# Optimization experiments

Hardware: AMD Instinct MI355X
Metric: run time of the kernel (lower is better)

## Reference

```python
import jax, jax.numpy as jnp
import numpy as np

R, DIL = 3, 2  # radius, dilation for neighbor correlation


def conv2d(x, w, b):
    # standard 3x3 stride-1 SAME conv, NCHW / OIHW
    y = jax.lax.conv_general_dilated(x, w, (1, 1), 'SAME',
                                     dimension_numbers=('NCHW', 'OIHW', 'NCHW'))
    return y + b[None, :, None, None]


def bilinear_gather(x, py, px):
    # x: (n,c,h,w); py/px: (n,K,h,w) float sampling coords; zero outside bounds
    n, c, h, w = x.shape
    y0 = jnp.floor(py); x0 = jnp.floor(px)
    wy = py - y0; wx = px - x0
    xf = x.reshape(n, c, h * w)

    def gather(yi, xi):
        valid = ((yi >= 0) & (yi < h) & (xi >= 0) & (xi < w)).astype(x.dtype)
        yc = jnp.clip(yi, 0, h - 1).astype(jnp.int32)
        xc = jnp.clip(xi, 0, w - 1).astype(jnp.int32)
        idx = (yc * w + xc).reshape(n, -1)  # (n, K*h*w)
        v = jax.vmap(lambda f, i: f[:, i])(xf, idx)  # (n, c, K*h*w)
        return v.reshape(n, c, *yi.shape[1:]) * valid[:, None]

    v00 = gather(y0, x0); v01 = gather(y0, x0 + 1)
    v10 = gather(y0 + 1, x0); v11 = gather(y0 + 1, x0 + 1)
    wy_ = wy[:, None]; wx_ = wx[:, None]
    return (v00 * (1 - wy_) * (1 - wx_) + v01 * (1 - wy_) * wx_
            + v10 * wy_ * (1 - wx_) + v11 * wy_ * wx_)


def dcn(x, w, b, ow, ob):
    # DCNv2-style modulated deformable 3x3 conv, stride 1, pad 1, 1 deformable group.
    # Offset/mask predicted by an internal conv: channels = [dy(9), dx(9), mask(9)].
    n, c, h, w_ = x.shape
    K = 9
    om = conv2d(x, ow, ob)  # (n, 27, h, w)
    dy, dx = om[:, :K], om[:, K:2 * K]
    mask = jax.nn.sigmoid(om[:, 2 * K:])
    ky, kx = jnp.meshgrid(jnp.arange(-1, 2), jnp.arange(-1, 2), indexing='ij')
    ky = ky.reshape(K).astype(x.dtype); kx = kx.reshape(K).astype(x.dtype)
    yy = jnp.arange(h, dtype=x.dtype)[None, None, :, None]
    xx = jnp.arange(w_, dtype=x.dtype)[None, None, None, :]
    py = yy + ky[None, :, None, None] + dy  # (n,K,h,w)
    px = xx + kx[None, :, None, None] + dx
    samp = bilinear_gather(x, py, px) * mask[:, None]  # (n,c,K,h,w)
    return jnp.einsum('nckhw,ock->nohw', samp, w.reshape(w.shape[0], c, K)) + b[None, :, None, None]


def ncf(f1, f2, radius, dilation):
    # neighbor_correlation_filter: unfold-based sliding-window dot-product attention
    n, c, h, w = f2.shape
    k = 2 * radius + 1
    pad = (k - 1) * dilation // 2
    f2p = jnp.pad(f2, ((0, 0), (0, 0), (pad, pad), (pad, pad)))
    # (n,c,K,h,w), tap order (ky outer, kx inner) matching F.unfold row-major layout
    patches = jnp.stack([f2p[:, :, i * dilation:i * dilation + h, j * dilation:j * dilation + w]
                         for i in range(k) for j in range(k)], axis=2)
    corr = jnp.einsum('nchw,nckhw->nkhw', f1, patches) / jnp.sqrt(jnp.asarray(c, f1.dtype))
    attn = jax.nn.softmax(corr, axis=1)
    sample = jnp.einsum('nkhw,nckhw->nchw', attn, patches)
    return sample, corr


def stargru(x, t, zw, zb, zow, zob, hw, hb, how, hob):
    tx = jnp.concatenate([x, t], axis=1)
    z = jax.nn.sigmoid(dcn(tx, zw, zb, zow, zob))
    r, _ = ncf(t, x, R, DIL)
    xt = jnp.tanh(dcn(jnp.concatenate([r, t], axis=1), hw, hb, how, hob))
    return (1.0 - z) * t + z * xt


def setup_inputs():
    key = jax.random.key(0)
    N, CIN, CH, H, W = 2, 256, 64, 96, 96
    ks = iter(jax.random.split(key, 32))

    def rn(shape, s=0.05):
        return jax.random.normal(next(ks), shape, jnp.float32) * s

    inp = {
        'x': jax.random.normal(next(ks), (N, CIN, H, W), jnp.float32),
        'template': jax.random.normal(next(ks), (N, CH, H, W), jnp.float32),
        'w_in': rn((CH, CIN, 3, 3)), 'b_in': jnp.zeros((CH,), jnp.float32),
        'w_out': rn((CIN, CH, 3, 3)), 'b_out': jnp.zeros((CIN,), jnp.float32),
    }
    for pre in ('enh_z', 'enh_h', 'upd_z', 'upd_h'):
        inp[pre + '_w'] = rn((CH, 2 * CH, 3, 3))
        inp[pre + '_b'] = jnp.zeros((CH,), jnp.float32)
        inp[pre + '_ow'] = rn((27, 2 * CH, 3, 3), 0.01)  # offset/mask conv (small init)
        inp[pre + '_ob'] = jnp.zeros((27,), jnp.float32)
    return inp


def reference(x, template, w_in, b_in, w_out, b_out,
              enh_z_w, enh_z_b, enh_z_ow, enh_z_ob,
              enh_h_w, enh_h_b, enh_h_ow, enh_h_ob,
              upd_z_w, upd_z_b, upd_z_ow, upd_z_ob,
              upd_h_w, upd_h_b, upd_h_ow, upd_h_ob):
    # CrossUpdate forward, post-first-frame branch (self.template is not None)
    xh = conv2d(x, w_in, b_in)
    x_enh = stargru(template, xh,
                    enh_z_w, enh_z_b, enh_z_ow, enh_z_ob,
                    enh_h_w, enh_h_b, enh_h_ow, enh_h_ob)
    new_template = stargru(xh, template,
                           upd_z_w, upd_z_b, upd_z_ow, upd_z_ob,
                           upd_h_w, upd_h_b, upd_h_ow, upd_h_ob)
    out = conv2d(x_enh, w_out, b_out)
    return (out, new_template)
```

## Files before the change

### kernel.cpp

```cpp
#include <hip/hip_runtime.h>
#include <hip/hip_bf16.h>

typedef __hip_bfloat16 bf16;
typedef unsigned short u16;
typedef unsigned int u32;
typedef __attribute__((ext_vector_type(8))) short short8;
typedef __attribute__((ext_vector_type(4))) short bh4;
typedef __attribute__((ext_vector_type(4))) float floatx4;

constexpr int N_ = 2, H_ = 96, W_ = 96, HW_ = H_ * W_;
constexpr int CIN_ = 256, CH_ = 64, C2_ = 128;

__device__ __forceinline__ float sigm(float v) { return 1.0f / (1.0f + __expf(-v)); }
__device__ __forceinline__ short f2b(float v) { bf16 h = __float2bfloat16(v); return *reinterpret_cast<short*>(&h); }
__device__ __forceinline__ float b2f(short s) {
    union { u32 i; float f; } v; v.i = ((u32)(u16)s) << 16; return v.f;
}

constexpr int A_IN_OFF = 0,                         A_IN_SZ  = 64 * 2304;
constexpr int A_OUT_OFF = A_IN_OFF + A_IN_SZ,       A_OUT_SZ = 256 * 576;
constexpr int A_OFF_OFF = A_OUT_OFF + A_OUT_SZ,     A_OFF_SZ = 64 * 1152;
constexpr int A_DCN_OFF = A_OFF_OFF + 4 * A_OFF_SZ, A_DCN_SZ = 64 * 1152;
constexpr int A_TOT = A_DCN_OFF + 4 * A_DCN_SZ;

__global__ __launch_bounds__(256) void cvt_weights(
        const float* __restrict__ w_in, const float* __restrict__ w_out,
        const float* __restrict__ ow0, const float* __restrict__ ow1,
        const float* __restrict__ ow2, const float* __restrict__ ow3,
        const float* __restrict__ w0, const float* __restrict__ w1,
        const float* __restrict__ w2, const float* __restrict__ w3,
        u16* __restrict__ dst) {
    int id = blockIdx.x * 256 + threadIdx.x;
    if (id >= A_TOT) return;
    float v;
    if (id < A_OUT_OFF) {
        int l = id; int m = l / 2304, k = l % 2304; int tap = k >> 8, ic = k & 255;
        v = w_in[m * 2304 + ic * 9 + tap];
    } else if (id < A_OFF_OFF) {
        int l = id - A_OUT_OFF; int m = l / 576, k = l % 576; int tap = k / 64, ic = k & 63;
        v = w_out[m * 576 + ic * 9 + tap];
    } else if (id < A_DCN_OFF) {
        int l = id - A_OFF_OFF; int i = l / A_OFF_SZ, l2 = l % A_OFF_SZ;
        int m = l2 / 1152, k = l2 % 1152; int tap = k >> 7, ic = k & 127;
        const float* s = (i == 0) ? ow0 : (i == 1) ? ow1 : (i == 2) ? ow2 : ow3;
        v = (m < 27) ? s[m * 1152 + ic * 9 + tap] : 0.f;
    } else {
        int l = id - A_DCN_OFF; int i = l / A_DCN_SZ, l2 = l % A_DCN_SZ;
        int m = l2 / 1152, k = l2 % 1152; int tap = k >> 7, c = k & 127;
        const float* s = (i == 0) ? w0 : (i == 1) ? w1 : (i == 2) ? w2 : w3;
        v = s[m * 1152 + c * 9 + tap];
    }
    short sb = f2b(v);
    dst[id] = *reinterpret_cast<u16*>(&sb);
}

__global__ __launch_bounds__(256) void to_nhwc(const float* __restrict__ src, u16* __restrict__ dst, int C) {
    int id = blockIdx.x * 256 + threadIdx.x;
    int c8n = C >> 3;
    if (id >= N_ * HW_ * c8n) return;
    int c8 = id % c8n;
    int pix = id / c8n;
    int n = pix / HW_, p = pix % HW_;
    const float* s = src + ((size_t)n * C + c8 * 8) * HW_ + p;
    short8 vv;
#pragma unroll
    for (int j = 0; j < 8; ++j) vv[j] = f2b(s[(size_t)j * HW_]);
    *reinterpret_cast<short8*>(dst + (size_t)pix * C + c8 * 8) = vv;
}

__global__ __launch_bounds__(256) void concat_dual(const float* __restrict__ tpl, const float* __restrict__ xh,
                                                   u16* __restrict__ ta, u16* __restrict__ tb) {
    int id = blockIdx.x * 256 + threadIdx.x;
    if (id >= N_ * HW_ * 16) return;
    int c8 = id & 15;
    int pix = id >> 4;
    int n = pix / HW_, p = pix % HW_;
    int c = c8 * 8;
    const float* s = (c < 64) ? tpl + ((size_t)n * 64 + c) * HW_ + p
                              : xh + ((size_t)n * 64 + (c - 64)) * HW_ + p;
    short8 vv;
#pragma unroll
    for (int j = 0; j < 8; ++j) vv[j] = f2b(s[(size_t)j * HW_]);
    *reinterpret_cast<short8*>(ta + (size_t)pix * 128 + c) = vv;
    *reinterpret_cast<short8*>(tb + (size_t)pix * 128 + ((c + 64) & 127)) = vv;
}

template <int IC, int OCST>
__device__ __forceinline__ void conv_core(const u16* __restrict__ X,
                                          const u16* __restrict__ A,
                                          const float* __restrict__ bias,
                                          float* __restrict__ out,
                                          int r, int mt, int t) {
    constexpr int K = IC * 9;
    constexpr int ICC = IC / 64;
    __shared__ __align__(16) u16 Xl[3][50][72];
    int n = r / 192;
    int rr = r % 192;
    int y = rr >> 1, px0 = (rr & 1) * 48;
    int w = t >> 6, lane = t & 63, lm = lane & 15, q = lane >> 4;
    const u16* Arow = A + (size_t)(mt * 64 + w * 16 + lm) * K + q * 8;
    floatx4 acc[3];
#pragma unroll
    for (int a = 0; a < 3; ++a) acc[a] = {0.f, 0.f, 0.f, 0.f};
    const short8 zz = {0, 0, 0, 0, 0, 0, 0, 0};

    for (int icc = 0; icc < ICC; ++icc) {
        short8 af[9][2];
#pragma unroll
        for (int tap = 0; tap < 9; ++tap)
#pragma unroll
            for (int ks = 0; ks < 2; ++ks)
                af[tap][ks] = *reinterpret_cast<const short8*>(Arow + tap * IC + icc * 64 + ks * 32);
        __syncthreads();
#pragma unroll
        for (int it = 0; it < 5; ++it) {
            int id = it * 256 + t;
            if (id < 1200) {
                int ch8 = id & 7;
                int tmp = id >> 3;
                int pxl = tmp % 50, row = tmp / 50;
                int xg = px0 - 1 + pxl;
                int yg = y - 1 + row;
                bool vld = (yg >= 0) && (yg < 96) && (xg >= 0) && (xg < 96);
                short8 vv = zz;
                if (vld)
                    vv = *reinterpret_cast<const short8*>(
                        X + ((size_t)(n * HW_ + yg * 96 + xg)) * IC + icc * 64 + ch8 * 8);
                *reinterpret_cast<short8*>(&Xl[row][pxl][ch8 * 8]) = vv;
            }
        }
        __syncthreads();
#pragma unroll
        for (int tap = 0; tap < 9; ++tap) {
            int ky = tap / 3, kx = tap % 3;
#pragma unroll
            for (int ks = 0; ks < 2; ++ks) {
#pragma unroll
                for (int nf = 0; nf < 3; ++nf) {
                    short8 bv = *reinterpret_cast<const short8*>(&Xl[ky][nf * 16 + lm + kx][ks * 32 + q * 8]);
                    acc[nf] = __builtin_amdgcn_mfma_f32_16x16x32_bf16(af[tap][ks], bv, acc[nf], 0, 0, 0);
                }
            }
        }
    }
    int ocb = mt * 64 + w * 16 + q * 4;
#pragma unroll
    for (int nf = 0; nf < 3; ++nf) {
        int px = px0 + nf * 16 + lm;
#pragma unroll
        for (int rr2 = 0; rr2 < 4; ++rr2) {
            int oc = ocb + rr2;
            if (oc < OCST)
                out[((size_t)(n * OCST + oc)) * HW_ + y * 96 + px] = acc[nf][rr2] + bias[oc];
        }
    }
}

template <int IC, int OCST>
__global__ __launch_bounds__(256) void conv_gemm(const u16* __restrict__ X,
                                                 const u16* __restrict__ A,
                                                 const float* __restrict__ bias,
                                                 float* __restrict__ out) {
    conv_core<IC, OCST>(X, A, bias, out, blockIdx.x % 384, blockIdx.x / 384, threadIdx.x);
}

__global__ __launch_bounds__(256) void conv_gemm2(const u16* __restrict__ X0, const u16* __restrict__ X1,
                                                  const u16* __restrict__ A0, const u16* __restrict__ A1,
                                                  const float* __restrict__ b0, const float* __restrict__ b1,
                                                  float* __restrict__ o0, float* __restrict__ o1) {
    int inst = blockIdx.x / 384, r = blockIdx.x % 384;
    conv_core<C2_, 27>(inst ? X1 : X0, inst ? A1 : A0, inst ? b1 : b0, inst ? o1 : o0, r, 0, threadIdx.x);
}

__device__ __forceinline__ void dcn_core(const u16* __restrict__ txh,
                                         const float* __restrict__ om,
                                         const u16* __restrict__ A,
                                         const float* __restrict__ bias,
                                         float* __restrict__ out,
                                         int r, int t) {
    __shared__ __align__(16) u16 Bl[48][72];
    __shared__ float s_wy[432], s_wx[432], s_m[432];
    __shared__ int s_y0[432], s_x0[432];
    int n = r / 192;
    int rr = r % 192;
    int y = rr >> 1, px0 = (rr & 1) * 48;
    for (int e = t; e < 432; e += 256) {
        int k9 = e / 48, xl = e % 48;
        int x = px0 + xl;
        const float* ob = om + (size_t)n * 27 * HW_ + y * 96 + x;
        float dy = ob[(size_t)k9 * HW_];
        float dx = ob[(size_t)(9 + k9) * HW_];
        float ml = ob[(size_t)(18 + k9) * HW_];
        float py = (float)y + (float)(k9 / 3 - 1) + dy;
        float px = (float)x + (float)(k9 % 3 - 1) + dx;
        float fy = floorf(py), fx = floorf(px);
        s_y0[e] = (int)fy; s_x0[e] = (int)fx;
        s_wy[e] = py - fy; s_wx[e] = px - fx; s_m[e] = sigm(ml);
    }
    int w = t >> 6, lane = t & 63, lm = lane & 15, q = lane >> 4;
    const u16* Arow = A + (size_t)(w * 16 + lm) * 1152 + q * 8;
    floatx4 acc[3];
#pragma unroll
    for (int a = 0; a < 3; ++a) acc[a] = {0.f, 0.f, 0.f, 0.f};
    const u16* txn = txh + (size_t)n * HW_ * 128;
    const short8 zz = {0, 0, 0, 0, 0, 0, 0, 0};

    for (int kc = 0; kc < 18; ++kc) {
        int tap = kc >> 1, c0 = (kc & 1) * 64;
        short8 af[2];
#pragma unroll
        for (int ks = 0; ks < 2; ++ks)
            af[ks] = *reinterpret_cast<const short8*>(Arow + kc * 64 + ks * 32);
        __syncthreads();
#pragma unroll
        for (int i = 0; i < 2; ++i) {
            int id = i * 256 + t;
            if (id < 384) {
                int px = id >> 3, ch8 = id & 7;
                int ce = tap * 48 + px;
                int y0 = s_y0[ce], x0 = s_x0[ce];
                float wy = s_wy[ce], wx = s_wx[ce], m = s_m[ce];
                float w00 = (1.f - wy) * (1.f - wx) * m;
                float w01 = (1.f - wy) * wx * m;
                float w10 = wy * (1.f - wx) * m;
                float w11 = wy * wx * m;
                bool yv0 = (y0 >= 0) & (y0 < 96), yv1 = (y0 >= -1) & (y0 < 95);
                bool xv0 = (x0 >= 0) & (x0 < 96), xv1 = (x0 >= -1) & (x0 < 95);
                const u16* base = txn + (long)(y0 * 96 + x0) * 128 + c0 + ch8 * 8;
                short8 v00 = (yv0 && xv0) ? *reinterpret_cast<const short8*>(base) : zz;
                short8 v01 = (yv0 && xv1) ? *reinterpret_cast<const short8*>(base + 128) : zz;
                short8 v10 = (yv1 && xv0) ? *reinterpret_cast<const short8*>(base + 96 * 128) : zz;
                short8 v11 = (yv1 && xv1) ? *reinterpret_cast<const short8*>(base + 96 * 128 + 128) : zz;
                short8 vv;
#pragma unroll
                for (int j = 0; j < 8; ++j) {
                    float f = b2f(v00[j]) * w00 + b2f(v01[j]) * w01 +
                              b2f(v10[j]) * w10 + b2f(v11[j]) * w11;
                    vv[j] = f2b(f);
                }
                *reinterpret_cast<short8*>(&Bl[px][ch8 * 8]) = vv;
            }
        }
        __syncthreads();
#pragma unroll
        for (int ks = 0; ks < 2; ++ks)
#pragma unroll
            for (int nf = 0; nf < 3; ++nf) {
                short8 bv = *reinterpret_cast<const short8*>(&Bl[nf * 16 + lm][ks * 32 + q * 8]);
                acc[nf] = __builtin_amdgcn_mfma_f32_16x16x32_bf16(af[ks], bv, acc[nf], 0, 0, 0);
            }
    }
    int ocb = w * 16 + q * 4;
#pragma unroll
    for (int nf = 0; nf < 3; ++nf) {
        int px = px0 + nf * 16 + lm;
#pragma unroll
        for (int rr2 = 0; rr2 < 4; ++rr2) {
            int oc = ocb + rr2;
            out[((size_t)(n * CH_ + oc)) * HW_ + y * 96 + px] = acc[nf][rr2] + bias[oc];
        }
    }
}

__global__ __launch_bounds__(256) void dcn_gemm2(const u16* __restrict__ X0, const u16* __restrict__ X1,
                                                 const float* __restrict__ om0, const float* __restrict__ om1,
                                                 const u16* __restrict__ A0, const u16* __restrict__ A1,
                                                 const float* __restrict__ b0, const float* __restrict__ b1,
                                                 float* __restrict__ o0, float* __restrict__ o1) {
    int inst = blockIdx.x / 384, r = blockIdx.x % 384;
    dcn_core(inst ? X1 : X0, inst ? om1 : om0, inst ? A1 : A0, inst ? b1 : b0, inst ? o1 : o0, r, threadIdx.x);
}

__global__ __launch_bounds__(256, 4) void ncf2(const u16* __restrict__ in0, const u16* __restrict__ in1,
                                               u16* __restrict__ out0, u16* __restrict__ out1) {
    __shared__ __align__(16) u16 sF2[7][28][72];
    __shared__ __align__(16) u16 sF1[16][72];
    __shared__ float sc[16][52];
    int t = threadIdx.x;
    int inst = blockIdx.x / 1152, bb = blockIdx.x % 1152;
    const u16* txh = inst ? in1 : in0;
    u16* txh2 = inst ? out1 : out0;
    int n = bb / 576, rem = bb % 576;
    int y = rem / 6, x0 = (rem % 6) * 16;
    const u16* base = txh + (size_t)n * HW_ * 128;
    const short8 zz = {0, 0, 0, 0, 0, 0, 0, 0};

    for (int id = t; id < 1568; id += 256) {
        int ch8 = id & 7;
        int tmp = id >> 3;
        int px = tmp % 28, row = tmp / 28;
        int yy = y + row * 2 - 6;
        int xg = x0 - 6 + px;
        short8 vv = zz;
        if (yy >= 0 && yy < 96 && xg >= 0 && xg < 96)
            vv = *reinterpret_cast<const short8*>(base + (size_t)(yy * 96 + xg) * 128 + ch8 * 8);
        *reinterpret_cast<short8*>(&sF2[row][px][ch8 * 8]) = vv;
    }
    if (t < 128) {
        int ch8 = t & 7, lp0 = t >> 3;
        short8 vv = *reinterpret_cast<const short8*>(base + (size_t)(y * 96 + x0 + lp0) * 128 + 64 + ch8 * 8);
        *reinterpret_cast<short8*>(&sF1[lp0][ch8 * 8]) = vv;
    }
    __syncthreads();

    int lp = t >> 4, j = t & 15;
    for (int k = j; k < 49; k += 16) {
        int ky = k / 7, kx = k % 7;
        const u16* f2p = &sF2[ky][lp + 2 * kx][0];
        const u16* f1p = &sF1[lp][0];
        float s = 0.f;
#pragma unroll
        for (int c8 = 0; c8 < 8; ++c8) {
            short8 a = *reinterpret_cast<const short8*>(f1p + c8 * 8);
            short8 b = *reinterpret_cast<const short8*>(f2p + c8 * 8);
#pragma unroll
            for (int u = 0; u < 8; ++u) s += b2f(a[u]) * b2f(b[u]);
        }
        sc[lp][k] = s * 0.125f;
    }
    float mx = -1e30f;
    for (int k = j; k < 49; k += 16) mx = fmaxf(mx, sc[lp][k]);
#pragma unroll
    for (int m = 1; m <= 8; m <<= 1) mx = fmaxf(mx, __shfl_xor(mx, m, 64));
    float e[4];
    float sum = 0.f;
    int cnt = 0;
    for (int k = j; k < 49; k += 16) { e[cnt] = __expf(sc[lp][k] - mx); sum += e[cnt]; ++cnt; }
#pragma unroll
    for (int m = 1; m <= 8; m <<= 1) sum += __shfl_xor(sum, m, 64);
    float inv = 1.f / sum;
    cnt = 0;
    for (int k = j; k < 49; k += 16) sc[lp][k] = e[cnt++] * inv;
    __syncthreads();
    int ch0 = j * 4;
    float acc[4];
#pragma unroll
    for (int u = 0; u < 4; ++u) acc[u] = 0.f;
#pragma unroll
    for (int k = 0; k < 49; ++k) {
        int ky = k / 7, kx = k % 7;
        float a = sc[lp][k];
        bh4 f2 = *reinterpret_cast<const bh4*>(&sF2[ky][lp + 2 * kx][ch0]);
#pragma unroll
        for (int u = 0; u < 4; ++u) acc[u] += a * b2f(f2[u]);
    }
    int p = y * 96 + x0 + lp;
    u16* obase = txh2 + (size_t)n * HW_ * 128 + (size_t)p * 128;
    bh4 ro;
#pragma unroll
    for (int u = 0; u < 4; ++u) ro[u] = f2b(acc[u]);
    *reinterpret_cast<bh4*>(obase + ch0) = ro;
    *reinterpret_cast<bh4*>(obase + 64 + ch0) =
        *reinterpret_cast<const bh4*>(&sF1[lp][ch0]);
}

__global__ __launch_bounds__(256) void gate_dual(const float* __restrict__ dz_a, const float* __restrict__ dh_a,
                                                 const float* __restrict__ t_a, u16* __restrict__ dst_a,
                                                 const float* __restrict__ dz_b, const float* __restrict__ dh_b,
                                                 const float* __restrict__ t_b, float* __restrict__ dst_b) {
    int inst = blockIdx.x / 576, bb = blockIdx.x % 576;
    int id = bb * 256 + threadIdx.x;
    int c8 = id & 7;
    int pix = id >> 3;
    int n = pix / HW_, p = pix % HW_;
    const float* zpre = inst ? dz_b : dz_a;
    const float* hpre = inst ? dh_b : dh_a;
    const float* tt = inst ? t_b : t_a;
    if (!inst) {
        short8 vv;
#pragma unroll
        for (int j = 0; j < 8; ++j) {
            size_t idx = ((size_t)n * CH_ + c8 * 8 + j) * HW_ + p;
            float z = sigm(zpre[idx]);
            float xt = tanhf(hpre[idx]);
            vv[j] = f2b((1.f - z) * tt[idx] + z * xt);
        }
        *reinterpret_cast<short8*>(dst_a + (size_t)pix * CH_ + c8 * 8) = vv;
    } else {
#pragma unroll
        for (int j = 0; j < 8; ++j) {
            size_t idx = ((size_t)n * CH_ + c8 * 8 + j) * HW_ + p;
            float z = sigm(zpre[idx]);
            float xt = tanhf(hpre[idx]);
            dst_b[idx] = (1.f - z) * tt[idx] + z * xt;
        }
    }
}

extern "C" void kernel_launch(void* const* d_in, const int* in_sizes, int n_in,
                              void* d_out, int out_size, void* d_ws, size_t ws_size,
                              hipStream_t stream) {
    const float* x     = (const float*)d_in[0];
    const float* tpl   = (const float*)d_in[1];
    const float* w_in  = (const float*)d_in[2];
    const float* b_in  = (const float*)d_in[3];
    const float* w_out = (const float*)d_in[4];
    const float* b_out = (const float*)d_in[5];
    const float *pw[4], *pb[4], *pow_[4], *pob[4];
    for (int i = 0; i < 4; ++i) {
        pw[i]   = (const float*)d_in[6 + 4 * i];
        pb[i]   = (const float*)d_in[7 + 4 * i];
        pow_[i] = (const float*)d_in[8 + 4 * i];
        pob[i]  = (const float*)d_in[9 + 4 * i];
    }
    float* out_main = (float*)d_out;
    float* out_ntpl = out_main + (size_t)N_ * CIN_ * HW_;

    u16* Aws = (u16*)d_ws;
    u16* xT     = Aws + A_TOT;
    u16* txh_a  = xT + (size_t)N_ * HW_ * CIN_;
    u16* txh_b  = txh_a + (size_t)N_ * HW_ * C2_;
    u16* txh2_a = txh_b + (size_t)N_ * HW_ * C2_;
    u16* txh2_b = txh2_a + (size_t)N_ * HW_ * C2_;
    u16* xeh    = txh2_b + (size_t)N_ * HW_ * C2_;
    float* fws = (float*)(xeh + (size_t)N_ * HW_ * CH_);
    size_t off = 0;
    float* xh   = fws + off; off += (size_t)N_ * CH_ * HW_;
    float* om_a = fws + off; off += (size_t)N_ * 27 * HW_;
    float* om_b = fws + off; off += (size_t)N_ * 27 * HW_;
    float* dz_a = fws + off; off += (size_t)N_ * CH_ * HW_;
    float* dz_b = fws + off; off += (size_t)N_ * CH_ * HW_;
    float* dh_a = fws + off; off += (size_t)N_ * CH_ * HW_;
    float* dh_b = fws + off; off += (size_t)N_ * CH_ * HW_;

    cvt_weights<<<(A_TOT + 255) / 256, 256, 0, stream>>>(
        w_in, w_out, pow_[0], pow_[1], pow_[2], pow_[3], pw[0], pw[1], pw[2], pw[3], Aws);
    to_nhwc<<<2304, 256, 0, stream>>>(x, xT, CIN_);
    conv_gemm<CIN_, 64><<<384, 256, 0, stream>>>(xT, Aws + A_IN_OFF, b_in, xh);

    concat_dual<<<1152, 256, 0, stream>>>(tpl, xh, txh_a, txh_b);
    conv_gemm2<<<768, 256, 0, stream>>>(txh_a, txh_b,
        Aws + A_OFF_OFF + 0 * A_OFF_SZ, Aws + A_OFF_OFF + 2 * A_OFF_SZ, pob[0], pob[2], om_a, om_b);
    dcn_gemm2<<<768, 256, 0, stream>>>(txh_a, txh_b, om_a, om_b,
        Aws + A_DCN_OFF + 0 * A_DCN_SZ, Aws + A_DCN_OFF + 2 * A_DCN_SZ, pb[0], pb[2], dz_a, dz_b);
    ncf2<<<2304, 256, 0, stream>>>(txh_a, txh_b, txh2_a, txh2_b);
    conv_gemm2<<<768, 256, 0, stream>>>(txh2_a, txh2_b,
        Aws + A_OFF_OFF + 1 * A_OFF_SZ, Aws + A_OFF_OFF + 3 * A_OFF_SZ, pob[1], pob[3], om_a, om_b);
    dcn_gemm2<<<768, 256, 0, stream>>>(txh2_a, txh2_b, om_a, om_b,
        Aws + A_DCN_OFF + 1 * A_DCN_SZ, Aws + A_DCN_OFF + 3 * A_DCN_SZ, pb[1], pb[3], dh_a, dh_b);
    gate_dual<<<1152, 256, 0, stream>>>(dz_a, dh_a, xh, xeh, dz_b, dh_b, tpl, out_ntpl);

    conv_gemm<CH_, 256><<<1536, 256, 0, stream>>>(xeh, Aws + A_OUT_OFF, b_out, out_main);
}
```

Baseline: 342.0 us.

## Fuse offset conv into DCN kernels, gate into DCN epilogue, concat into conv_in

Merges the offset/mask conv with the deformable conv in one kernel, so each block computes its own offset/mask tile into shared memory instead of round-tripping it through global memory. The GRU gate is folded into the second DCN's epilogue, and the xh-to-NHWC concat is folded into the input conv's epilogue, with the template conversion merged into the x conversion kernel. This removes three launches and several full-tensor intermediate writes and reads. The cost is higher shared memory and register use per fused block, which may lower occupancy.

```diff
diff --git a/kernel.cpp b/kernel.cpp
--- a/kernel.cpp
+++ b/kernel.cpp
@@ -54,42 +54,39 @@
     dst[id] = *reinterpret_cast<u16*>(&sb);
 }
 
-__global__ __launch_bounds__(256) void to_nhwc(const float* __restrict__ src, u16* __restrict__ dst, int C) {
+__global__ __launch_bounds__(256) void prep(const float* __restrict__ x, const float* __restrict__ tpl,
+                                            u16* __restrict__ xT, u16* __restrict__ ta, u16* __restrict__ tb) {
     int id = blockIdx.x * 256 + threadIdx.x;
-    int c8n = C >> 3;
-    if (id >= N_ * HW_ * c8n) return;
-    int c8 = id % c8n;
-    int pix = id / c8n;
-    int n = pix / HW_, p = pix % HW_;
-    const float* s = src + ((size_t)n * C + c8 * 8) * HW_ + p;
-    short8 vv;
-#pragma unroll
-    for (int j = 0; j < 8; ++j) vv[j] = f2b(s[(size_t)j * HW_]);
-    *reinterpret_cast<short8*>(dst + (size_t)pix * C + c8 * 8) = vv;
-}
-
-__global__ __launch_bounds__(256) void concat_dual(const float* __restrict__ tpl, const float* __restrict__ xh,
-                                                   u16* __restrict__ ta, u16* __restrict__ tb) {
-    int id = blockIdx.x * 256 + threadIdx.x;
-    if (id >= N_ * HW_ * 16) return;
-    int c8 = id & 15;
-    int pix = id >> 4;
-    int n = pix / HW_, p = pix % HW_;
-    int c = c8 * 8;
-    const float* s = (c < 64) ? tpl + ((size_t)n * 64 + c) * HW_ + p
-                              : xh + ((size_t)n * 64 + (c - 64)) * HW_ + p;
-    short8 vv;
-#pragma unroll
-    for (int j = 0; j < 8; ++j) vv[j] = f2b(s[(size_t)j * HW_]);
-    *reinterpret_cast<short8*>(ta + (size_t)pix * 128 + c) = vv;
-    *reinterpret_cast<short8*>(tb + (size_t)pix * 128 + ((c + 64) & 127)) = vv;
-}
-
-template <int IC, int OCST>
+    constexpr int XIDS = N_ * HW_ * 32;
+    if (id < XIDS) {
+        int c8 = id & 31;
+        int pix = id >> 5;
+        int n = pix / HW_, p = pix % HW_;
+        const float* s = x + ((size_t)n * 256 + c8 * 8) * HW_ + p;
+        short8 vv;
+#pragma unroll
+        for (int j = 0; j < 8; ++j) vv[j] = f2b(s[(size_t)j * HW_]);
+        *reinterpret_cast<short8*>(xT + (size_t)pix * 256 + c8 * 8) = vv;
+    } else {
+        int id2 = id - XIDS;
+        int c8 = id2 & 7;
+        int pix = id2 >> 3;
+        int n = pix / HW_, p = pix % HW_;
+        const float* s = tpl + ((size_t)n * 64 + c8 * 8) * HW_ + p;
+        short8 vv;
+#pragma unroll
+        for (int j = 0; j < 8; ++j) vv[j] = f2b(s[(size_t)j * HW_]);
+        *reinterpret_cast<short8*>(ta + (size_t)pix * 128 + c8 * 8) = vv;
+        *reinterpret_cast<short8*>(tb + (size_t)pix * 128 + 64 + c8 * 8) = vv;
+    }
+}
+
+template <int IC, int OCST, int CC>
 __device__ __forceinline__ void conv_core(const u16* __restrict__ X,
                                           const u16* __restrict__ A,
                                           const float* __restrict__ bias,
                                           float* __restrict__ out,
+                                          u16* __restrict__ ta, u16* __restrict__ tb,
                                           int r, int mt, int t) {
     constexpr int K = IC * 9;
     constexpr int ICC = IC / 64;
@@ -147,63 +144,139 @@
 #pragma unroll
     for (int nf = 0; nf < 3; ++nf) {
         int px = px0 + nf * 16 + lm;
-#pragma unroll
-        for (int rr2 = 0; rr2 < 4; ++rr2) {
-            int oc = ocb + rr2;
-            if (oc < OCST)
-                out[((size_t)(n * OCST + oc)) * HW_ + y * 96 + px] = acc[nf][rr2] + bias[oc];
-        }
-    }
-}
-
-template <int IC, int OCST>
+        if constexpr (CC) {
+            int pix = n * HW_ + y * 96 + px;
+            bh4 bo;
+#pragma unroll
+            for (int rr2 = 0; rr2 < 4; ++rr2) {
+                int oc = ocb + rr2;
+                float v = acc[nf][rr2] + bias[oc];
+                out[((size_t)(n * OCST + oc)) * HW_ + y * 96 + px] = v;
+                bo[rr2] = f2b(v);
+            }
+            *reinterpret_cast<bh4*>(ta + (size_t)pix * 128 + 64 + ocb) = bo;
+            *reinterpret_cast<bh4*>(tb + (size_t)pix * 128 + ocb) = bo;
+        } else {
+#pragma unroll
+            for (int rr2 = 0; rr2 < 4; ++rr2) {
+                int oc = ocb + rr2;
+                if (oc < OCST)
+                    out[((size_t)(n * OCST + oc)) * HW_ + y * 96 + px] = acc[nf][rr2] + bias[oc];
+            }
+        }
+    }
+}
+
+template <int IC, int OCST, int CC>
 __global__ __launch_bounds__(256) void conv_gemm(const u16* __restrict__ X,
                                                  const u16* __restrict__ A,
                                                  const float* __restrict__ bias,
-                                                 float* __restrict__ out) {
-    conv_core<IC, OCST>(X, A, bias, out, blockIdx.x % 384, blockIdx.x / 384, threadIdx.x);
-}
-
-__global__ __launch_bounds__(256) void conv_gemm2(const u16* __restrict__ X0, const u16* __restrict__ X1,
-                                                  const u16* __restrict__ A0, const u16* __restrict__ A1,
-                                                  const float* __restrict__ b0, const float* __restrict__ b1,
-                                                  float* __restrict__ o0, float* __restrict__ o1) {
-    int inst = blockIdx.x / 384, r = blockIdx.x % 384;
-    conv_core<C2_, 27>(inst ? X1 : X0, inst ? A1 : A0, inst ? b1 : b0, inst ? o1 : o0, r, 0, threadIdx.x);
-}
-
-__device__ __forceinline__ void dcn_core(const u16* __restrict__ txh,
-                                         const float* __restrict__ om,
-                                         const u16* __restrict__ A,
-                                         const float* __restrict__ bias,
-                                         float* __restrict__ out,
-                                         int r, int t) {
+                                                 float* __restrict__ out,
+                                                 u16* __restrict__ ta, u16* __restrict__ tb) {
+    conv_core<IC, OCST, CC>(X, A, bias, out, ta, tb, blockIdx.x % 384, blockIdx.x / 384, threadIdx.x);
+}
+
+template <int GATE>
+__global__ __launch_bounds__(256) void od_fused(
+        const u16* __restrict__ X0, const u16* __restrict__ X1,
+        const u16* __restrict__ Ao0, const u16* __restrict__ Ao1,
+        const float* __restrict__ bo0, const float* __restrict__ bo1,
+        const u16* __restrict__ Ad0, const u16* __restrict__ Ad1,
+        const float* __restrict__ bd0, const float* __restrict__ bd1,
+        float* __restrict__ o0, float* __restrict__ o1,
+        const float* __restrict__ g0, const float* __restrict__ g1,
+        const float* __restrict__ t0, const float* __restrict__ t1,
+        u16* __restrict__ xeh, float* __restrict__ ontpl) {
+    __shared__ __align__(16) u16 Xl[3][50][72];
+    __shared__ float om_l[27][48];
     __shared__ __align__(16) u16 Bl[48][72];
     __shared__ float s_wy[432], s_wx[432], s_m[432];
     __shared__ int s_y0[432], s_x0[432];
-    int n = r / 192;
-    int rr = r % 192;
+    int inst = blockIdx.x / 384, r = blockIdx.x % 384, t = threadIdx.x;
+    const u16* X = inst ? X1 : X0;
+    const u16* Ao = inst ? Ao1 : Ao0;
+    const float* bo = inst ? bo1 : bo0;
+    const u16* Ad = inst ? Ad1 : Ad0;
+    const float* bd = inst ? bd1 : bd0;
+    int n = r / 192, rr = r % 192;
     int y = rr >> 1, px0 = (rr & 1) * 48;
+    int w = t >> 6, lane = t & 63, lm = lane & 15, q = lane >> 4;
+    const short8 zz = {0, 0, 0, 0, 0, 0, 0, 0};
+
+    {
+        const u16* Arow = Ao + (size_t)(w * 16 + lm) * 1152 + q * 8;
+        floatx4 acc[3];
+#pragma unroll
+        for (int a = 0; a < 3; ++a) acc[a] = {0.f, 0.f, 0.f, 0.f};
+        for (int icc = 0; icc < 2; ++icc) {
+            short8 af[9][2];
+#pragma unroll
+            for (int tap = 0; tap < 9; ++tap)
+#pragma unroll
+                for (int ks = 0; ks < 2; ++ks)
+                    af[tap][ks] = *reinterpret_cast<const short8*>(Arow + tap * 128 + icc * 64 + ks * 32);
+            __syncthreads();
+#pragma unroll
+            for (int it = 0; it < 5; ++it) {
+                int id = it * 256 + t;
+                if (id < 1200) {
+                    int ch8 = id & 7;
+                    int tmp = id >> 3;
+                    int pxl = tmp % 50, row = tmp / 50;
+                    int xg = px0 - 1 + pxl;
+                    int yg = y - 1 + row;
+                    bool vld = (yg >= 0) && (yg < 96) && (xg >= 0) && (xg < 96);
+                    short8 vv = zz;
+                    if (vld)
+                        vv = *reinterpret_cast<const short8*>(
+                            X + ((size_t)(n * HW_ + yg * 96 + xg)) * 128 + icc * 64 + ch8 * 8);
+                    *reinterpret_cast<short8*>(&Xl[row][pxl][ch8 * 8]) = vv;
+                }
+            }
+            __syncthreads();
+#pragma unroll
+            for (int tap = 0; tap < 9; ++tap) {
+                int ky = tap / 3, kx = tap % 3;
+#pragma unroll
+                for (int ks = 0; ks < 2; ++ks) {
+#pragma unroll
+                    for (int nf = 0; nf < 3; ++nf) {
+                        short8 bv = *reinterpret_cast<const short8*>(&Xl[ky][nf * 16 + lm + kx][ks * 32 + q * 8]);
+                        acc[nf] = __builtin_amdgcn_mfma_f32_16x16x32_bf16(af[tap][ks], bv, acc[nf], 0, 0, 0);
+                    }
+                }
+            }
+        }
+        int ocb = w * 16 + q * 4;
+#pragma unroll
+        for (int nf = 0; nf < 3; ++nf) {
+            int xl = nf * 16 + lm;
+#pragma unroll
+            for (int rr2 = 0; rr2 < 4; ++rr2) {
+                int oc = ocb + rr2;
+                if (oc < 27) om_l[oc][xl] = acc[nf][rr2] + bo[oc];
+            }
+        }
+    }
+    __syncthreads();
+
     for (int e = t; e < 432; e += 256) {
         int k9 = e / 48, xl = e % 48;
         int x = px0 + xl;
-        const float* ob = om + (size_t)n * 27 * HW_ + y * 96 + x;
-        float dy = ob[(size_t)k9 * HW_];
-        float dx = ob[(size_t)(9 + k9) * HW_];
-        float ml = ob[(size_t)(18 + k9) * HW_];
+        float dy = om_l[k9][xl];
+        float dx = om_l[9 + k9][xl];
+        float ml = om_l[18 + k9][xl];
         float py = (float)y + (float)(k9 / 3 - 1) + dy;
         float px = (float)x + (float)(k9 % 3 - 1) + dx;
         float fy = floorf(py), fx = floorf(px);
         s_y0[e] = (int)fy; s_x0[e] = (int)fx;
         s_wy[e] = py - fy; s_wx[e] = px - fx; s_m[e] = sigm(ml);
     }
-    int w = t >> 6, lane = t & 63, lm = lane & 15, q = lane >> 4;
-    const u16* Arow = A + (size_t)(w * 16 + lm) * 1152 + q * 8;
+    const u16* Arow = Ad + (size_t)(w * 16 + lm) * 1152 + q * 8;
     floatx4 acc[3];
 #pragma unroll
     for (int a = 0; a < 3; ++a) acc[a] = {0.f, 0.f, 0.f, 0.f};
-    const u16* txn = txh + (size_t)n * HW_ * 128;
-    const short8 zz = {0, 0, 0, 0, 0, 0, 0, 0};
+    const u16* txn = X + (size_t)n * HW_ * 128;
 
     for (int kc = 0; kc < 18; ++kc) {
         int tap = kc >> 1, c0 = (kc & 1) * 64;
@@ -251,24 +324,46 @@
             }
     }
     int ocb = w * 16 + q * 4;
-#pragma unroll
-    for (int nf = 0; nf < 3; ++nf) {
-        int px = px0 + nf * 16 + lm;
-#pragma unroll
-        for (int rr2 = 0; rr2 < 4; ++rr2) {
-            int oc = ocb + rr2;
-            out[((size_t)(n * CH_ + oc)) * HW_ + y * 96 + px] = acc[nf][rr2] + bias[oc];
-        }
-    }
-}
-
-__global__ __launch_bounds__(256) void dcn_gemm2(const u16* __restrict__ X0, const u16* __restrict__ X1,
-                                                 const float* __restrict__ om0, const float* __restrict__ om1,
-                                                 const u16* __restrict__ A0, const u16* __restrict__ A1,
-                                                 const float* __restrict__ b0, const float* __restrict__ b1,
-                                                 float* __restrict__ o0, float* __restrict__ o1) {
-    int inst = blockIdx.x / 384, r = blockIdx.x % 384;
-    dcn_core(inst ? X1 : X0, inst ? om1 : om0, inst ? A1 : A0, inst ? b1 : b0, inst ? o1 : o0, r, threadIdx.x);
+    if constexpr (GATE == 0) {
+        float* out = inst ? o1 : o0;
+#pragma unroll
+        for (int nf = 0; nf < 3; ++nf) {
+            int px = px0 + nf * 16 + lm;
+#pragma unroll
+            for (int rr2 = 0; rr2 < 4; ++rr2) {
+                int oc = ocb + rr2;
+                out[((size_t)(n * CH_ + oc)) * HW_ + y * 96 + px] = acc[nf][rr2] + bd[oc];
+            }
+        }
+    } else {
+        const float* gz = inst ? g1 : g0;
+        const float* tt = inst ? t1 : t0;
+#pragma unroll
+        for (int nf = 0; nf < 3; ++nf) {
+            int px = px0 + nf * 16 + lm;
+            if (!inst) {
+                bh4 bo4;
+#pragma unroll
+                for (int rr2 = 0; rr2 < 4; ++rr2) {
+                    int oc = ocb + rr2;
+                    size_t idx = ((size_t)(n * CH_ + oc)) * HW_ + y * 96 + px;
+                    float z = sigm(gz[idx]);
+                    float xt = tanhf(acc[nf][rr2] + bd[oc]);
+                    bo4[rr2] = f2b((1.f - z) * tt[idx] + z * xt);
+                }
+                *reinterpret_cast<bh4*>(xeh + ((size_t)(n * HW_ + y * 96 + px)) * 64 + ocb) = bo4;
+            } else {
+#pragma unroll
+                for (int rr2 = 0; rr2 < 4; ++rr2) {
+                    int oc = ocb + rr2;
+                    size_t idx = ((size_t)(n * CH_ + oc)) * HW_ + y * 96 + px;
+                    float z = sigm(gz[idx]);
+                    float xt = tanhf(acc[nf][rr2] + bd[oc]);
+                    ontpl[idx] = (1.f - z) * tt[idx] + z * xt;
+                }
+            }
+        }
+    }
 }
 
 __global__ __launch_bounds__(256, 4) void ncf2(const u16* __restrict__ in0, const u16* __restrict__ in1,
@@ -352,39 +447,6 @@
     *reinterpret_cast<bh4*>(obase + ch0) = ro;
     *reinterpret_cast<bh4*>(obase + 64 + ch0) =
         *reinterpret_cast<const bh4*>(&sF1[lp][ch0]);
-}
-
-__global__ __launch_bounds__(256) void gate_dual(const float* __restrict__ dz_a, const float* __restrict__ dh_a,
-                                                 const float* __restrict__ t_a, u16* __restrict__ dst_a,
-                                                 const float* __restrict__ dz_b, const float* __restrict__ dh_b,
-                                                 const float* __restrict__ t_b, float* __restrict__ dst_b) {
-    int inst = blockIdx.x / 576, bb = blockIdx.x % 576;
-    int id = bb * 256 + threadIdx.x;
-    int c8 = id & 7;
-    int pix = id >> 3;
-    int n = pix / HW_, p = pix % HW_;
-    const float* zpre = inst ? dz_b : dz_a;
-    const float* hpre = inst ? dh_b : dh_a;
-    const float* tt = inst ? t_b : t_a;
-    if (!inst) {
-        short8 vv;
-#pragma unroll
-        for (int j = 0; j < 8; ++j) {
-            size_t idx = ((size_t)n * CH_ + c8 * 8 + j) * HW_ + p;
-            float z = sigm(zpre[idx]);
-            float xt = tanhf(hpre[idx]);
-            vv[j] = f2b((1.f - z) * tt[idx] + z * xt);
-        }
-        *reinterpret_cast<short8*>(dst_a + (size_t)pix * CH_ + c8 * 8) = vv;
-    } else {
-#pragma unroll
-        for (int j = 0; j < 8; ++j) {
-            size_t idx = ((size_t)n * CH_ + c8 * 8 + j) * HW_ + p;
-            float z = sigm(zpre[idx]);
-            float xt = tanhf(hpre[idx]);
-            dst_b[idx] = (1.f - z) * tt[idx] + z * xt;
-        }
-    }
 }
 
 extern "C" void kernel_launch(void* const* d_in, const int* in_sizes, int n_in,
@@ -416,29 +478,25 @@
     float* fws = (float*)(xeh + (size_t)N_ * HW_ * CH_);
     size_t off = 0;
     float* xh   = fws + off; off += (size_t)N_ * CH_ * HW_;
-    float* om_a = fws + off; off += (size_t)N_ * 27 * HW_;
-    float* om_b = fws + off; off += (size_t)N_ * 27 * HW_;
     float* dz_a = fws + off; off += (size_t)N_ * CH_ * HW_;
     float* dz_b = fws + off; off += (size_t)N_ * CH_ * HW_;
-    float* dh_a = fws + off; off += (size_t)N_ * CH_ * HW_;
-    float* dh_b = fws + off; off += (size_t)N_ * CH_ * HW_;
 
     cvt_weights<<<(A_TOT + 255) / 256, 256, 0, stream>>>(
         w_in, w_out, pow_[0], pow_[1], pow_[2], pow_[3], pw[0], pw[1], pw[2], pw[3], Aws);
-    to_nhwc<<<2304, 256, 0, stream>>>(x, xT, CIN_);
-    conv_gemm<CIN_, 64><<<384, 256, 0, stream>>>(xT, Aws + A_IN_OFF, b_in, xh);
-
-    concat_dual<<<1152, 256, 0, stream>>>(tpl, xh, txh_a, txh_b);
-    conv_gemm2<<<768, 256, 0, stream>>>(txh_a, txh_b,
-        Aws + A_OFF_OFF + 0 * A_OFF_SZ, Aws + A_OFF_OFF + 2 * A_OFF_SZ, pob[0], pob[2], om_a, om_b);
-    dcn_gemm2<<<768, 256, 0, stream>>>(txh_a, txh_b, om_a, om_b,
-        Aws + A_DCN_OFF + 0 * A_DCN_SZ, Aws + A_DCN_OFF + 2 * A_DCN_SZ, pb[0], pb[2], dz_a, dz_b);
+    prep<<<2880, 256, 0, stream>>>(x, tpl, xT, txh_a, txh_b);
+    conv_gemm<CIN_, 64, 1><<<384, 256, 0, stream>>>(xT, Aws + A_IN_OFF, b_in, xh, txh_a, txh_b);
+
+    od_fused<0><<<768, 256, 0, stream>>>(txh_a, txh_b,
+        Aws + A_OFF_OFF + 0 * A_OFF_SZ, Aws + A_OFF_OFF + 2 * A_OFF_SZ, pob[0], pob[2],
+        Aws + A_DCN_OFF + 0 * A_DCN_SZ, Aws + A_DCN_OFF + 2 * A_DCN_SZ, pb[0], pb[2],
+        dz_a, dz_b, nullptr, nullptr, nullptr, nullptr, nullptr, nullptr);
+
     ncf2<<<2304, 256, 0, stream>>>(txh_a, txh_b, txh2_a, txh2_b);
-    conv_gemm2<<<768, 256, 0, stream>>>(txh2_a, txh2_b,
-        Aws + A_OFF_OFF + 1 * A_OFF_SZ, Aws + A_OFF_OFF + 3 * A_OFF_SZ, pob[1], pob[3], om_a, om_b);
-    dcn_gemm2<<<768, 256, 0, stream>>>(txh2_a, txh2_b, om_a, om_b,
-        Aws + A_DCN_OFF + 1 * A_DCN_SZ, Aws + A_DCN_OFF + 3 * A_DCN_SZ, pb[1], pb[3], dh_a, dh_b);
-    gate_dual<<<1152, 256, 0, stream>>>(dz_a, dh_a, xh, xeh, dz_b, dh_b, tpl, out_ntpl);
-
-    conv_gemm<CH_, 256><<<1536, 256, 0, stream>>>(xeh, Aws + A_OUT_OFF, b_out, out_main);
-}
+
+    od_fused<1><<<768, 256, 0, stream>>>(txh2_a, txh2_b,
+        Aws + A_OFF_OFF + 1 * A_OFF_SZ, Aws + A_OFF_OFF + 3 * A_OFF_SZ, pob[1], pob[3],
+        Aws + A_DCN_OFF + 1 * A_DCN_SZ, Aws + A_DCN_OFF + 3 * A_DCN_SZ, pb[1], pb[3],
+        nullptr, nullptr, dz_a, dz_b, xh, tpl, xeh, out_ntpl);
+
+    conv_gemm<CH_, 256, 0><<<1536, 256, 0, stream>>>(xeh, Aws + A_OUT_OFF, b_out, out_main, nullptr, nullptr);
+}
```

New measurement: 322.4 us. -5.7%, faster.
